# Kernel optimization log

Hardware: AMD Instinct MI355X
Metric: run time of the kernel (lower is better)

The kernel has to match this reference:

```python
import jax, jax.numpy as jnp
import numpy as np

NUM_CLASSES = 80
CONF_THRE = 0.2
NMS_THRE = 0.45
MAX_DET = 300   # fixed cap replacing torch's variable-length NMS output (padded + keep mask)
IMG = 640.0


def setup_inputs() -> dict:
    key = jax.random.key(0)
    k1, k2 = jax.random.split(key)
    pred = jax.random.uniform(k1, (32, 8400, 85), dtype=jnp.float32)
    # scale cx,cy,w,h to pixel range so IoU/NMS geometry is realistic
    pred = pred.at[..., :4].multiply(IMG)
    zone = jax.random.uniform(k2, (8, 2), dtype=jnp.float32) * IMG
    return {"prediction": pred, "zone": zone}


def _pairwise_iou(b):
    # b: [B, K, 4] in x1y1x2y2
    area = jnp.clip(b[..., 2] - b[..., 0], 0.0) * jnp.clip(b[..., 3] - b[..., 1], 0.0)
    lt = jnp.maximum(b[:, :, None, :2], b[:, None, :, :2])
    rb = jnp.minimum(b[:, :, None, 2:], b[:, None, :, 2:])
    wh = jnp.clip(rb - lt, 0.0)
    inter = wh[..., 0] * wh[..., 1]
    return inter / (area[:, :, None] + area[:, None, :] - inter + 1e-9)


def _postprocess(prediction):
    # decode cx,cy,w,h -> x1,y1,x2,y2
    xy = prediction[..., :2]
    wh = prediction[..., 2:4]
    boxes = jnp.concatenate([xy - wh * 0.5, xy + wh * 0.5], axis=-1)  # [B,N,4]
    obj = prediction[..., 4]                                           # [B,N]
    cls = prediction[..., 5:5 + NUM_CLASSES]
    class_conf = jnp.max(cls, axis=-1)                                 # [B,N]
    class_pred = jnp.argmax(cls, axis=-1)                              # [B,N]

    # confidence mask (obj * class_conf >= thre); invalid -> -inf so top_k drops them
    nms_score = obj * class_conf
    nms_score = jnp.where(nms_score >= CONF_THRE, nms_score, -jnp.inf)

    s, idx = jax.lax.top_k(nms_score, MAX_DET)                         # [B,K]
    b = jnp.take_along_axis(boxes, idx[..., None], axis=1)             # [B,K,4]

    # class-agnostic greedy NMS on score-sorted boxes (matches torchvision.ops.nms)
    iou = _pairwise_iou(b)                                             # [B,K,K]
    keep = jnp.isfinite(s)                                             # valid (passed conf) entries
    ar = jnp.arange(MAX_DET)
    def body(i, keep):
        sup = keep[:, i][:, None] & (iou[:, i, :] > NMS_THRE) & (ar > i)
        return keep & jnp.logical_not(sup)
    keep = jax.lax.fori_loop(0, MAX_DET, body, keep)

    obj_s = jnp.take_along_axis(obj, idx, axis=1)
    conf_s = jnp.take_along_axis(class_conf, idx, axis=1)
    cls_s = jnp.take_along_axis(class_pred, idx, axis=1).astype(jnp.int32)
    # extract_boxes_scores_and_classes: score = max over columns [obj, class_conf]
    scores = jnp.maximum(obj_s, conf_s)
    return b, scores, cls_s, keep


def _points_inside_zone(px, py, zone):
    # px, py: [B,K]; zone: [Z,2]. Ray-casting parity test (faithful to torch version).
    zr = jnp.roll(zone, shift=1, axis=0)
    xi, yi = zone[:, 0], zone[:, 1]
    xj, yj = zr[:, 0], zr[:, 1]
    pyb = py[..., None]  # [B,K,1] vs [Z]
    pxb = px[..., None]
    gyi = yi > pyb
    gyj = yj > pyb
    gx = (xj - xi) * (pyb - yi) / (yj - yi) + xi
    inter = (gyi != gyj) & (gx > pxb)
    return (jnp.sum(inter.astype(jnp.int32), axis=-1) % 2) > 0


def reference(prediction, zone):
    b, scores, classes, keep = _postprocess(prediction)
    cx = (b[..., 0] + b[..., 2]) * 0.5
    cy = (b[..., 1] + b[..., 3]) * 0.5
    in_zone = _points_inside_zone(cx, cy, zone) & keep
    centers_yx = jnp.stack([cy, cx], axis=-1)                          # [B,K,2]
    boxes_yxyx = jnp.stack([b[..., 1], b[..., 0], b[..., 3], b[..., 2]], axis=-1)
    return boxes_yxyx, in_zone, scores, classes, centers_yx, keep
```

## Files before the change

### kernel.cpp

```cpp
#include <hip/hip_runtime.h>
#include <stdint.h>

typedef unsigned long long ull;

#define NA 8400
#define NB 32
#define KTOP 300
#define NC 80
#define CH 9
#define NCOPY 16
#define HSTRIDE 257

#define O1 38400
#define O2 48000
#define O3 57600
#define O4 67200
#define O5 86400

__global__ __launch_bounds__(256) void score_kernel(const float* __restrict__ pred,
                                                    uint32_t* __restrict__ keys) {
    __shared__ float sP[128 * 85];
    const int blk = blockIdx.x;
    const float4* g4 = (const float4*)(pred + (size_t)blk * 128 * 85);
    float4* l4 = (float4*)sP;
    for (int i = threadIdx.x; i < (128 * 85 / 4); i += 256) l4[i] = g4[i];
    __syncthreads();
    const int t = threadIdx.x;
    if (t < 128) {
        const float* p = sP + t * 85;
        float obj = p[4];
        float b0 = p[5], b1 = p[6], b2 = p[7], b3 = p[8];
        #pragma unroll
        for (int c = 4; c < NC; c += 4) {
            b0 = fmaxf(b0, p[5 + c]);
            b1 = fmaxf(b1, p[6 + c]);
            b2 = fmaxf(b2, p[7 + c]);
            b3 = fmaxf(b3, p[8 + c]);
        }
        float best = fmaxf(fmaxf(b0, b1), fmaxf(b2, b3));
        float sc = obj * best;
        uint32_t u = (sc >= 0.2f) ? (__float_as_uint(sc) | 0x80000000u) : 0x007FFFFFu;
        keys[(size_t)blk * 128 + t] = u;
    }
}

__global__ __launch_bounds__(1024) void batch_kernel(const float* __restrict__ pred,
                                                     const float* __restrict__ zone,
                                                     const uint32_t* __restrict__ keys,
                                                     float* __restrict__ out) {
    #pragma clang fp contract(off)
    __shared__ float sB0[KTOP], sB1[KTOP], sB2[KTOP], sB3[KTOP];
    __shared__ ull sMask[KTOP * 5];
    __shared__ ull sSel[KTOP];
    __shared__ ull sSorted[KTOP];
    __shared__ uint32_t sH[NCOPY * HSTRIDE];
    __shared__ uint32_t sWTot[16];
    __shared__ uint32_t sBc[2];
    __shared__ uint32_t sRank[KTOP];
    __shared__ uint32_t sPar[KTOP];
    __shared__ ull sKeepF[5];
    __shared__ float sZone[16];

    const int b = blockIdx.x;
    const int t = threadIdx.x;
    const int lane = t & 63;
    const int wv = t >> 6;

    uint32_t myk[CH];
    const int beg = t * CH;
    #pragma unroll
    for (int e = 0; e < CH; ++e) {
        int idx = beg + e;
        myk[e] = (idx < NA) ? keys[(size_t)b * NA + idx] : 0u;
    }
    if (t < 16) sZone[t] = zone[t];
    if (t < KTOP) sRank[t] = 0u;

    uint32_t prefix = 0, r = KTOP;
    for (int round = 0; round < 4; ++round) {
        const int shift = 24 - 8 * round;
        for (int i = t; i < NCOPY * HSTRIDE; i += 1024) sH[i] = 0u;
        __syncthreads();
        const uint32_t pmask = (round == 0) ? 0u : (0xFFFFFFFFu << (shift + 8));
        const uint32_t pref = prefix & pmask;
        #pragma unroll
        for (int e = 0; e < CH; ++e) {
            uint32_t k = myk[e];
            if ((k & pmask) == pref)
                atomicAdd(&sH[wv * HSTRIDE + ((k >> shift) & 0xFFu)], 1u);
        }
        __syncthreads();
        if (wv == 0) {
            uint32_t v0 = 0, v1 = 0, v2 = 0, v3 = 0;
            #pragma unroll
            for (int c = 0; c < NCOPY; ++c) {
                const uint32_t* hc = &sH[c * HSTRIDE];
                v0 += hc[lane]; v1 += hc[64 + lane];
                v2 += hc[128 + lane]; v3 += hc[192 + lane];
            }
            uint32_t s0 = v0, s1 = v1, s2 = v2, s3 = v3;
            #pragma unroll
            for (int off = 1; off < 64; off <<= 1) {
                uint32_t o0 = __shfl_down(s0, off, 64), o1 = __shfl_down(s1, off, 64);
                uint32_t o2 = __shfl_down(s2, off, 64), o3 = __shfl_down(s3, off, 64);
                if (lane + off < 64) { s0 += o0; s1 += o1; s2 += o2; s3 += o3; }
            }
            uint32_t T1 = __shfl(s1, 0, 64), T2 = __shfl(s2, 0, 64), T3 = __shfl(s3, 0, 64);
            uint32_t S0 = s0 + T1 + T2 + T3;
            uint32_t S1 = s1 + T2 + T3;
            uint32_t S2 = s2 + T3;
            uint32_t S3 = s3;
            if (S0 >= r && S0 - v0 < r) { sBc[0] = prefix | ((uint32_t)lane << shift);         sBc[1] = r - (S0 - v0); }
            if (S1 >= r && S1 - v1 < r) { sBc[0] = prefix | ((uint32_t)(64  + lane) << shift); sBc[1] = r - (S1 - v1); }
            if (S2 >= r && S2 - v2 < r) { sBc[0] = prefix | ((uint32_t)(128 + lane) << shift); sBc[1] = r - (S2 - v2); }
            if (S3 >= r && S3 - v3 < r) { sBc[0] = prefix | ((uint32_t)(192 + lane) << shift); sBc[1] = r - (S3 - v3); }
        }
        __syncthreads();
        prefix = sBc[0]; r = sBc[1];
    }
    const uint32_t kth = prefix;
    const uint32_t rem = r;
    const uint32_t cntgt = KTOP - rem;

    {
        uint32_t gtc = 0, eqc = 0;
        #pragma unroll
        for (int e = 0; e < CH; ++e) {
            uint32_t k = myk[e];
            gtc += (k > kth) ? 1u : 0u;
            eqc += (k == kth) ? 1u : 0u;
        }
        uint32_t pack = (gtc << 16) | eqc;
        uint32_t ps = pack;
        #pragma unroll
        for (int off = 1; off < 64; off <<= 1) {
            uint32_t o = __shfl_up(ps, off, 64);
            if (lane >= off) ps += o;
        }
        if (lane == 63) sWTot[wv] = ps;
        __syncthreads();
        uint32_t excl = ps - pack;
        #pragma unroll
        for (int w2 = 0; w2 < 16; ++w2) if (w2 < wv) excl += sWTot[w2];
        uint32_t gtoff = excl >> 16;
        uint32_t eqoff = excl & 0xFFFFu;
        #pragma unroll
        for (int e = 0; e < CH; ++e) {
            uint32_t k = myk[e];
            uint32_t idx = (uint32_t)(beg + e);
            if (k > kth) {
                sSel[gtoff++] = ((ull)k << 32) | (ull)(0xFFFFFFFFu - idx);
            } else if (k == kth) {
                if (eqoff < rem)
                    sSel[cntgt + eqoff] = ((ull)k << 32) | (ull)(0xFFFFFFFFu - idx);
                eqoff++;
            }
        }
        __syncthreads();
    }

    for (int p2 = t; p2 < KTOP * 4; p2 += 1024) {
        const int i = p2 >> 2;
        const int q = p2 & 3;
        const ull my = sSel[i];
        const int j0 = q * 75, j1 = j0 + 75;
        uint32_t cnt = 0;
        for (int j = j0; j < j1; ++j)
            cnt += (sSel[j] > my) ? 1u : 0u;
        if (cnt) atomicAdd(&sRank[i], cnt);
    }
    __syncthreads();
    if (t < KTOP) sSorted[sRank[t]] = sSel[t];
    __syncthreads();

    const size_t bo = (size_t)b * KTOP;
    if (t < 2 * KTOP) {
        const int row = t >> 1;
        const int half = t & 1;
        const uint32_t a = 0xFFFFFFFFu - (uint32_t)sSorted[row];
        const float* p = pred + ((size_t)b * NA + a) * 85;
        const int cbase = half * 40;
        float v0 = p[5 + cbase], v1 = p[6 + cbase], v2 = p[7 + cbase], v3 = p[8 + cbase];
        int   c0 = cbase, c1 = cbase + 1, c2 = cbase + 2, c3 = cbase + 3;
        #pragma unroll
        for (int c = 4; c < 40; c += 4) {
            float w0 = p[5 + cbase + c],     w1 = p[6 + cbase + c];
            float w2 = p[7 + cbase + c],     w3 = p[8 + cbase + c];
            if (w0 > v0) { v0 = w0; c0 = cbase + c; }
            if (w1 > v1) { v1 = w1; c1 = cbase + c + 1; }
            if (w2 > v2) { v2 = w2; c2 = cbase + c + 2; }
            if (w3 > v3) { v3 = w3; c3 = cbase + c + 3; }
        }
        float bv = v0; int bc = c0;
        if (v1 > bv || (v1 == bv && c1 < bc)) { bv = v1; bc = c1; }
        if (v2 > bv || (v2 == bv && c2 < bc)) { bv = v2; bc = c2; }
        if (v3 > bv || (v3 == bv && c3 < bc)) { bv = v3; bc = c3; }
        float pv = __shfl_xor(bv, 1, 64);
        int   pc = __shfl_xor(bc, 1, 64);
        if (half == 0) {
            if (pv > bv) { bv = pv; bc = pc; }
            float x = p[0], y = p[1], w = p[2], h = p[3], obj = p[4];
            float hw = w * 0.5f, hh = h * 0.5f;
            float x1 = x - hw, y1 = y - hh, x2 = x + hw, y2 = y + hh;
            sB0[row] = x1; sB1[row] = y1; sB2[row] = x2; sB3[row] = y2;
            out[(bo + row) * 4 + 0] = y1;
            out[(bo + row) * 4 + 1] = x1;
            out[(bo + row) * 4 + 2] = y2;
            out[(bo + row) * 4 + 3] = x2;
            out[O4 + (bo + row) * 2 + 0] = (y1 + y2) * 0.5f;
            out[O4 + (bo + row) * 2 + 1] = (x1 + x2) * 0.5f;
            out[O2 + bo + row] = fmaxf(obj, bv);
            out[O3 + bo + row] = (float)bc;
        }
    }
    __syncthreads();

    for (int p2 = t; p2 < KTOP * 5; p2 += 1024) {
        const int role = p2 / KTOP;
        const int i = p2 - role * KTOP;
        const int j0 = role * 64;
        int jmax = j0 + 64; if (jmax > KTOP) jmax = KTOP;
        float x1 = sB0[i], y1 = sB1[i], x2 = sB2[i], y2 = sB3[i];
        float ai = fmaxf(x2 - x1, 0.0f) * fmaxf(y2 - y1, 0.0f);
        ull bits = 0ull;
        for (int j = j0; j < jmax; ++j) {
            float bx1 = sB0[j], by1 = sB1[j], bx2 = sB2[j], by2 = sB3[j];
            float aj = fmaxf(bx2 - bx1, 0.0f) * fmaxf(by2 - by1, 0.0f);
            float iw = fminf(x2, bx2) - fmaxf(x1, bx1); iw = fmaxf(iw, 0.0f);
            float ih = fminf(y2, by2) - fmaxf(y1, by1); ih = fmaxf(ih, 0.0f);
            float inter = iw * ih;
            float den = ai + aj;
            den = den - inter;
            den = den + 1e-9f;
            float iou = inter / den;
            if (j > i && iou > 0.45f) bits |= (1ull << (j - j0));
        }
        sMask[i * 5 + role] = bits;
    }
    __syncthreads();

    if (wv == 0) {
        ull rm[5][5];
        ull kw[5];
        #pragma unroll
        for (int w = 0; w < 5; ++w) {
            int i = w * 64 + lane;
            bool f = (i < KTOP) && (((uint32_t)(sSorted[i] >> 32)) > 0x007FFFFFu);
            kw[w] = __ballot(f);
            #pragma unroll
            for (int ww = 0; ww < 5; ++ww)
                rm[w][ww] = (i < KTOP) ? sMask[i * 5 + ww] : 0ull;
        }
        #pragma unroll
        for (int w = 0; w < 5; ++w) {
            ull cur = kw[w];
            while (cur) {
                int ib = __builtin_ctzll(cur);
                ull m0 = __shfl(rm[w][0], ib);
                ull m1 = __shfl(rm[w][1], ib);
                ull m2 = __shfl(rm[w][2], ib);
                ull m3 = __shfl(rm[w][3], ib);
                ull m4 = __shfl(rm[w][4], ib);
                kw[0] &= ~m0; kw[1] &= ~m1; kw[2] &= ~m2; kw[3] &= ~m3; kw[4] &= ~m4;
                ull done = (ib == 63) ? 0ull : (~0ull << (ib + 1));
                cur = kw[w] & done;
            }
        }
        if (lane == 0) {
            #pragma unroll
            for (int w = 0; w < 5; ++w) sKeepF[w] = kw[w];
        }
    } else if (t >= 512 && t < 512 + KTOP) {
        const int i = t - 512;
        float cy = (sB1[i] + sB3[i]) * 0.5f;
        float cx = (sB0[i] + sB2[i]) * 0.5f;
        int cnt = 0;
        #pragma unroll
        for (int e = 0; e < 8; ++e) {
            float xi = sZone[2 * e], yi = sZone[2 * e + 1];
            int ep = (e + 7) & 7;
            float xj = sZone[2 * ep], yj = sZone[2 * ep + 1];
            bool gyi = yi > cy, gyj = yj > cy;
            if (gyi != gyj) {
                float gx = (xj - xi) * (cy - yi) / (yj - yi) + xi;
                if (gx > cx) cnt++;
            }
        }
        sPar[i] = (uint32_t)(cnt & 1);
    }
    __syncthreads();

    if (t < KTOP) {
        int kp = (int)((sKeepF[t >> 6] >> (t & 63)) & 1ull);
        int inz = (sPar[t] && kp) ? 1 : 0;
        out[O1 + bo + t] = (float)inz;
        out[O5 + bo + t] = (float)kp;
    }
}

extern "C" void kernel_launch(void* const* d_in, const int* in_sizes, int n_in,
                              void* d_out, int out_size, void* d_ws, size_t ws_size,
                              hipStream_t stream) {
    const float* pred = (const float*)d_in[0];
    const float* zone = (const float*)d_in[1];
    float* out = (float*)d_out;
    uint32_t* keys = (uint32_t*)d_ws;

    score_kernel<<<(NB * NA) / 128, 256, 0, stream>>>(pred, keys);
    batch_kernel<<<NB, 1024, 0, stream>>>(pred, zone, keys, out);
}
```

Before: 205.3 us.

## Split per-batch kernel into select, prep, and finish kernels via workspace

The single per-batch kernel is split into three launches. A select kernel stages keys in LDS and does the radix top-k. A prep kernel uses two blocks per batch, one gathering class argmax and writing outputs, the other building the IoU suppression mask. A finish kernel runs the greedy NMS and the zone test. This doubles the block count for the gather and IoU phases, which previously ran serially in one block, at the cost of extra launches and global workspace round-trips.

After: 209.1 us. About the same (+1.9%).

```diff
diff --git a/kernel.cpp b/kernel.cpp
--- a/kernel.cpp
+++ b/kernel.cpp
@@ -8,6 +8,7 @@
 #define KTOP 300
 #define NC 80
 #define CH 9
+#define NKPAD 9216
 #define NCOPY 16
 #define HSTRIDE 257
 
@@ -16,6 +17,9 @@
 #define O3 57600
 #define O4 67200
 #define O5 86400
+
+#define WS_BATCH_BASE (2u << 20)
+#define WS_BATCH_STRIDE 16384
 
 __global__ __launch_bounds__(256) void score_kernel(const float* __restrict__ pred,
                                                     uint32_t* __restrict__ keys) {
@@ -44,38 +48,31 @@
     }
 }
 
-__global__ __launch_bounds__(1024) void batch_kernel(const float* __restrict__ pred,
-                                                     const float* __restrict__ zone,
-                                                     const uint32_t* __restrict__ keys,
-                                                     float* __restrict__ out) {
-    #pragma clang fp contract(off)
-    __shared__ float sB0[KTOP], sB1[KTOP], sB2[KTOP], sB3[KTOP];
-    __shared__ ull sMask[KTOP * 5];
+__global__ __launch_bounds__(1024) void select_kernel(const uint32_t* __restrict__ keys,
+                                                      uint8_t* __restrict__ ws) {
+    __shared__ uint32_t sKeys[NKPAD];
     __shared__ ull sSel[KTOP];
     __shared__ ull sSorted[KTOP];
     __shared__ uint32_t sH[NCOPY * HSTRIDE];
     __shared__ uint32_t sWTot[16];
     __shared__ uint32_t sBc[2];
     __shared__ uint32_t sRank[KTOP];
-    __shared__ uint32_t sPar[KTOP];
-    __shared__ ull sKeepF[5];
-    __shared__ float sZone[16];
 
     const int b = blockIdx.x;
     const int t = threadIdx.x;
     const int lane = t & 63;
     const int wv = t >> 6;
 
-    uint32_t myk[CH];
+    {
+        const uint4* g4 = (const uint4*)(keys + (size_t)b * NA);
+        uint4* l4 = (uint4*)sKeys;
+        for (int i = t; i < NA / 4; i += 1024) l4[i] = g4[i];
+        for (int i = NA + t; i < NKPAD; i += 1024) sKeys[i] = 0u;
+    }
+    if (t < KTOP) sRank[t] = 0u;
+    __syncthreads();
+
     const int beg = t * CH;
-    #pragma unroll
-    for (int e = 0; e < CH; ++e) {
-        int idx = beg + e;
-        myk[e] = (idx < NA) ? keys[(size_t)b * NA + idx] : 0u;
-    }
-    if (t < 16) sZone[t] = zone[t];
-    if (t < KTOP) sRank[t] = 0u;
-
     uint32_t prefix = 0, r = KTOP;
     for (int round = 0; round < 4; ++round) {
         const int shift = 24 - 8 * round;
@@ -83,11 +80,12 @@
         __syncthreads();
         const uint32_t pmask = (round == 0) ? 0u : (0xFFFFFFFFu << (shift + 8));
         const uint32_t pref = prefix & pmask;
+        uint32_t* hw = &sH[wv * HSTRIDE];
         #pragma unroll
         for (int e = 0; e < CH; ++e) {
-            uint32_t k = myk[e];
+            uint32_t k = sKeys[beg + e];
             if ((k & pmask) == pref)
-                atomicAdd(&sH[wv * HSTRIDE + ((k >> shift) & 0xFFu)], 1u);
+                atomicAdd(&hw[(k >> shift) & 0xFFu], 1u);
         }
         __syncthreads();
         if (wv == 0) {
@@ -126,7 +124,7 @@
         uint32_t gtc = 0, eqc = 0;
         #pragma unroll
         for (int e = 0; e < CH; ++e) {
-            uint32_t k = myk[e];
+            uint32_t k = sKeys[beg + e];
             gtc += (k > kth) ? 1u : 0u;
             eqc += (k == kth) ? 1u : 0u;
         }
@@ -146,7 +144,7 @@
         uint32_t eqoff = excl & 0xFFFFu;
         #pragma unroll
         for (int e = 0; e < CH; ++e) {
-            uint32_t k = myk[e];
+            uint32_t k = sKeys[beg + e];
             uint32_t idx = (uint32_t)(beg + e);
             if (k > kth) {
                 sSel[gtoff++] = ((ull)k << 32) | (ull)(0xFFFFFFFFu - idx);
@@ -173,79 +171,122 @@
     if (t < KTOP) sSorted[sRank[t]] = sSel[t];
     __syncthreads();
 
+    ull* selW = (ull*)(ws + WS_BATCH_BASE + (size_t)b * WS_BATCH_STRIDE);
+    if (t < KTOP) selW[t] = sSorted[t];
+}
+
+__global__ __launch_bounds__(1024) void prep_kernel(const float* __restrict__ pred,
+                                                    uint8_t* __restrict__ ws,
+                                                    float* __restrict__ out) {
+    #pragma clang fp contract(off)
+    __shared__ float sB0[KTOP], sB1[KTOP], sB2[KTOP], sB3[KTOP];
+    const int b = blockIdx.y;
+    const int t = threadIdx.x;
+    const ull* sel = (const ull*)(ws + WS_BATCH_BASE + (size_t)b * WS_BATCH_STRIDE);
     const size_t bo = (size_t)b * KTOP;
-    if (t < 2 * KTOP) {
-        const int row = t >> 1;
-        const int half = t & 1;
-        const uint32_t a = 0xFFFFFFFFu - (uint32_t)sSorted[row];
-        const float* p = pred + ((size_t)b * NA + a) * 85;
-        const int cbase = half * 40;
-        float v0 = p[5 + cbase], v1 = p[6 + cbase], v2 = p[7 + cbase], v3 = p[8 + cbase];
-        int   c0 = cbase, c1 = cbase + 1, c2 = cbase + 2, c3 = cbase + 3;
-        #pragma unroll
-        for (int c = 4; c < 40; c += 4) {
-            float w0 = p[5 + cbase + c],     w1 = p[6 + cbase + c];
-            float w2 = p[7 + cbase + c],     w3 = p[8 + cbase + c];
-            if (w0 > v0) { v0 = w0; c0 = cbase + c; }
-            if (w1 > v1) { v1 = w1; c1 = cbase + c + 1; }
-            if (w2 > v2) { v2 = w2; c2 = cbase + c + 2; }
-            if (w3 > v3) { v3 = w3; c3 = cbase + c + 3; }
-        }
-        float bv = v0; int bc = c0;
-        if (v1 > bv || (v1 == bv && c1 < bc)) { bv = v1; bc = c1; }
-        if (v2 > bv || (v2 == bv && c2 < bc)) { bv = v2; bc = c2; }
-        if (v3 > bv || (v3 == bv && c3 < bc)) { bv = v3; bc = c3; }
-        float pv = __shfl_xor(bv, 1, 64);
-        int   pc = __shfl_xor(bc, 1, 64);
-        if (half == 0) {
-            if (pv > bv) { bv = pv; bc = pc; }
-            float x = p[0], y = p[1], w = p[2], h = p[3], obj = p[4];
+
+    if (blockIdx.x == 0) {
+        if (t < 2 * KTOP) {
+            const int row = t >> 1;
+            const int half = t & 1;
+            const uint32_t a = 0xFFFFFFFFu - (uint32_t)sel[row];
+            const float* p = pred + ((size_t)b * NA + a) * 85;
+            const int cbase = half * 40;
+            float v0 = p[5 + cbase], v1 = p[6 + cbase], v2 = p[7 + cbase], v3 = p[8 + cbase];
+            int   c0 = cbase, c1 = cbase + 1, c2 = cbase + 2, c3 = cbase + 3;
+            #pragma unroll
+            for (int c = 4; c < 40; c += 4) {
+                float w0 = p[5 + cbase + c],     w1 = p[6 + cbase + c];
+                float w2 = p[7 + cbase + c],     w3 = p[8 + cbase + c];
+                if (w0 > v0) { v0 = w0; c0 = cbase + c; }
+                if (w1 > v1) { v1 = w1; c1 = cbase + c + 1; }
+                if (w2 > v2) { v2 = w2; c2 = cbase + c + 2; }
+                if (w3 > v3) { v3 = w3; c3 = cbase + c + 3; }
+            }
+            float bv = v0; int bc = c0;
+            if (v1 > bv || (v1 == bv && c1 < bc)) { bv = v1; bc = c1; }
+            if (v2 > bv || (v2 == bv && c2 < bc)) { bv = v2; bc = c2; }
+            if (v3 > bv || (v3 == bv && c3 < bc)) { bv = v3; bc = c3; }
+            float pv = __shfl_xor(bv, 1, 64);
+            int   pc = __shfl_xor(bc, 1, 64);
+            if (half == 0) {
+                if (pv > bv) { bv = pv; bc = pc; }
+                float x = p[0], y = p[1], w = p[2], h = p[3], obj = p[4];
+                float hw = w * 0.5f, hh = h * 0.5f;
+                float x1 = x - hw, y1 = y - hh, x2 = x + hw, y2 = y + hh;
+                out[(bo + row) * 4 + 0] = y1;
+                out[(bo + row) * 4 + 1] = x1;
+                out[(bo + row) * 4 + 2] = y2;
+                out[(bo + row) * 4 + 3] = x2;
+                out[O4 + (bo + row) * 2 + 0] = (y1 + y2) * 0.5f;
+                out[O4 + (bo + row) * 2 + 1] = (x1 + x2) * 0.5f;
+                out[O2 + bo + row] = fmaxf(obj, bv);
+                out[O3 + bo + row] = (float)bc;
+            }
+        }
+    } else {
+        if (t < KTOP) {
+            const uint32_t a = 0xFFFFFFFFu - (uint32_t)sel[t];
+            const float* p = pred + ((size_t)b * NA + a) * 85;
+            float x = p[0], y = p[1], w = p[2], h = p[3];
             float hw = w * 0.5f, hh = h * 0.5f;
-            float x1 = x - hw, y1 = y - hh, x2 = x + hw, y2 = y + hh;
-            sB0[row] = x1; sB1[row] = y1; sB2[row] = x2; sB3[row] = y2;
-            out[(bo + row) * 4 + 0] = y1;
-            out[(bo + row) * 4 + 1] = x1;
-            out[(bo + row) * 4 + 2] = y2;
-            out[(bo + row) * 4 + 3] = x2;
-            out[O4 + (bo + row) * 2 + 0] = (y1 + y2) * 0.5f;
-            out[O4 + (bo + row) * 2 + 1] = (x1 + x2) * 0.5f;
-            out[O2 + bo + row] = fmaxf(obj, bv);
-            out[O3 + bo + row] = (float)bc;
-        }
-    }
-    __syncthreads();
-
-    for (int p2 = t; p2 < KTOP * 5; p2 += 1024) {
-        const int role = p2 / KTOP;
-        const int i = p2 - role * KTOP;
-        const int j0 = role * 64;
-        int jmax = j0 + 64; if (jmax > KTOP) jmax = KTOP;
-        float x1 = sB0[i], y1 = sB1[i], x2 = sB2[i], y2 = sB3[i];
-        float ai = fmaxf(x2 - x1, 0.0f) * fmaxf(y2 - y1, 0.0f);
-        ull bits = 0ull;
-        for (int j = j0; j < jmax; ++j) {
-            float bx1 = sB0[j], by1 = sB1[j], bx2 = sB2[j], by2 = sB3[j];
-            float aj = fmaxf(bx2 - bx1, 0.0f) * fmaxf(by2 - by1, 0.0f);
-            float iw = fminf(x2, bx2) - fmaxf(x1, bx1); iw = fmaxf(iw, 0.0f);
-            float ih = fminf(y2, by2) - fmaxf(y1, by1); ih = fmaxf(ih, 0.0f);
-            float inter = iw * ih;
-            float den = ai + aj;
-            den = den - inter;
-            den = den + 1e-9f;
-            float iou = inter / den;
-            if (j > i && iou > 0.45f) bits |= (1ull << (j - j0));
-        }
-        sMask[i * 5 + role] = bits;
-    }
-    __syncthreads();
-
+            sB0[t] = x - hw; sB1[t] = y - hh; sB2[t] = x + hw; sB3[t] = y + hh;
+        }
+        __syncthreads();
+        ull* maskW = (ull*)(ws + WS_BATCH_BASE + (size_t)b * WS_BATCH_STRIDE + 2400);
+        for (int p2 = t; p2 < KTOP * 5; p2 += 1024) {
+            const int role = p2 / KTOP;
+            const int i = p2 - role * KTOP;
+            const int j0 = role * 64;
+            int jmax = j0 + 64; if (jmax > KTOP) jmax = KTOP;
+            float x1 = sB0[i], y1 = sB1[i], x2 = sB2[i], y2 = sB3[i];
+            float ai = fmaxf(x2 - x1, 0.0f) * fmaxf(y2 - y1, 0.0f);
+            ull bits = 0ull;
+            for (int j = j0; j < jmax; ++j) {
+                float bx1 = sB0[j], by1 = sB1[j], bx2 = sB2[j], by2 = sB3[j];
+                float aj = fmaxf(bx2 - bx1, 0.0f) * fmaxf(by2 - by1, 0.0f);
+                float iw = fminf(x2, bx2) - fmaxf(x1, bx1); iw = fmaxf(iw, 0.0f);
+                float ih = fminf(y2, by2) - fmaxf(y1, by1); ih = fmaxf(ih, 0.0f);
+                float inter = iw * ih;
+                float den = ai + aj;
+                den = den - inter;
+                den = den + 1e-9f;
+                float iou = inter / den;
+                if (j > i && iou > 0.45f) bits |= (1ull << (j - j0));
+            }
+            maskW[i * 5 + role] = bits;
+        }
+    }
+}
+
+__global__ __launch_bounds__(512) void finish_kernel(const float* __restrict__ zone,
+                                                     const uint8_t* __restrict__ ws,
+                                                     float* __restrict__ out) {
+    #pragma clang fp contract(off)
+    __shared__ ull sMask[KTOP * 5];
+    __shared__ ull sSel[KTOP];
+    __shared__ uint32_t sPar[KTOP];
+    __shared__ ull sKeepF[5];
+    __shared__ float sZone[16];
+    const int b = blockIdx.x;
+    const int t = threadIdx.x;
+    const int lane = t & 63;
+    const int wv = t >> 6;
+    const ull* selG = (const ull*)(ws + WS_BATCH_BASE + (size_t)b * WS_BATCH_STRIDE);
+    const ull* maskG = selG + KTOP;
+    for (int i = t; i < KTOP; i += 512) sSel[i] = selG[i];
+    for (int i = t; i < KTOP * 5; i += 512) sMask[i] = maskG[i];
+    if (t < 16) sZone[t] = zone[t];
+    __syncthreads();
+
+    const size_t bo = (size_t)b * KTOP;
     if (wv == 0) {
         ull rm[5][5];
         ull kw[5];
         #pragma unroll
         for (int w = 0; w < 5; ++w) {
             int i = w * 64 + lane;
-            bool f = (i < KTOP) && (((uint32_t)(sSorted[i] >> 32)) > 0x007FFFFFu);
+            bool f = (i < KTOP) && (((uint32_t)(sSel[i] >> 32)) > 0x007FFFFFu);
             kw[w] = __ballot(f);
             #pragma unroll
             for (int ww = 0; ww < 5; ++ww)
@@ -270,10 +311,10 @@
             #pragma unroll
             for (int w = 0; w < 5; ++w) sKeepF[w] = kw[w];
         }
-    } else if (t >= 512 && t < 512 + KTOP) {
-        const int i = t - 512;
-        float cy = (sB1[i] + sB3[i]) * 0.5f;
-        float cx = (sB0[i] + sB2[i]) * 0.5f;
+    } else if (t >= 64 && t < 64 + KTOP) {
+        const int i = t - 64;
+        float cy = out[O4 + (bo + i) * 2 + 0];
+        float cx = out[O4 + (bo + i) * 2 + 1];
         int cnt = 0;
         #pragma unroll
         for (int e = 0; e < 8; ++e) {
@@ -305,7 +346,10 @@
     const float* zone = (const float*)d_in[1];
     float* out = (float*)d_out;
     uint32_t* keys = (uint32_t*)d_ws;
+    uint8_t* ws = (uint8_t*)d_ws;
 
     score_kernel<<<(NB * NA) / 128, 256, 0, stream>>>(pred, keys);
-    batch_kernel<<<NB, 1024, 0, stream>>>(pred, zone, keys, out);
-}
+    select_kernel<<<NB, 1024, 0, stream>>>(keys, ws);
+    prep_kernel<<<dim3(2, NB), 1024, 0, stream>>>(pred, ws, out);
+    finish_kernel<<<NB, 512, 0, stream>>>(zone, ws, out);
+}
```
